# Kernel tuning notes

Hardware: AMD Instinct MI355X
Metric: run time of the kernel (lower is better)

Reference implementation:

```python
import jax, jax.numpy as jnp
import numpy as np

# Graph block sizes (outermost -> innermost), fixed fanout neighbor sampling
N0, N1, N2, N3 = 256000, 25600, 2560, 512
D_IN, D_H, D_OUT = 1024, 256, 19
FANOUTS = (10, 10, 5)


def _lin(key, d_in, d_out):
    return jax.random.normal(key, (d_in, d_out), jnp.float32) / np.sqrt(d_in)


def setup_inputs() -> dict:
    key = jax.random.key(0)
    ks = jax.random.split(key, 13)
    x = jax.random.normal(ks[0], (N0, D_IN), jnp.float32)
    # DGL block convention: dst nodes are the first n_dst src nodes, so
    # h_dst = h[:n_dst]. Neighbor tables index into the src node set.
    nbr0 = jax.random.randint(ks[1], (N1, FANOUTS[0]), 0, N0)
    nbr1 = jax.random.randint(ks[2], (N2, FANOUTS[1]), 0, N1)
    nbr2 = jax.random.randint(ks[3], (N3, FANOUTS[2]), 0, N2)
    return {
        "x": x, "nbr0": nbr0, "nbr1": nbr1, "nbr2": nbr2,
        "Wself0": _lin(ks[4], D_IN, D_H), "Wneigh0": _lin(ks[5], D_IN, D_H),
        "b0": jnp.zeros((D_H,), jnp.float32),
        "Wself1": _lin(ks[6], D_H, D_H), "Wneigh1": _lin(ks[7], D_H, D_H),
        "b1": jnp.zeros((D_H,), jnp.float32),
        "Wself2": _lin(ks[8], D_H, D_OUT), "Wneigh2": _lin(ks[9], D_H, D_OUT),
        "b2": jnp.zeros((D_OUT,), jnp.float32),
    }


def sage_layer(h, nbr, Wself, Wneigh, b):
    # SAGEConv('mean'): fc_self(h_dst) + fc_neigh(mean over sampled neighbors)
    n_dst = nbr.shape[0]
    h_neigh = jnp.mean(h[nbr], axis=1)  # [n_dst, fanout, d] -> [n_dst, d]
    return h[:n_dst] @ Wself + h_neigh @ Wneigh + b


def reference(x, nbr0, nbr1, nbr2,
              Wself0, Wneigh0, b0,
              Wself1, Wneigh1, b1,
              Wself2, Wneigh2, b2):
    # Dropout is identity in eval mode; activation = relu.
    h = jax.nn.relu(sage_layer(x, nbr0, Wself0, Wneigh0, b0))
    h = jax.nn.relu(sage_layer(h, nbr1, Wself1, Wneigh1, b1))
    return sage_layer(h, nbr2, Wself2, Wneigh2, b2)  # [N3, n_classes]
```

## Files before the change

### kernel.cpp

```cpp
#include <hip/hip_runtime.h>
#include <hip/hip_bf16.h>


typedef __attribute__((ext_vector_type(4))) float f32x4;
typedef __attribute__((ext_vector_type(8))) short s16x8;

__device__ __forceinline__ unsigned short f2bf_u16(float f) {
  unsigned int u = __float_as_uint(f);
  u += 0x7fffu + ((u >> 16) & 1u);
  return (unsigned short)(u >> 16);
}

__device__ __forceinline__ float bf2f(unsigned short u) {
  return __uint_as_float(((unsigned int)u) << 16);
}

__global__ void prep_wcat(const float* __restrict__ Wself,
                          const float* __restrict__ Wneigh,
                          unsigned short* __restrict__ Wt, int Khalf, int N) {
  int idx = blockIdx.x * 256 + threadIdx.x;
  int Kc = 2 * Khalf;
  if (idx >= N * Kc) return;
  int n = idx / Kc, k = idx - n * Kc;
  float v = (k < Khalf) ? Wself[(size_t)k * N + n] : Wneigh[(size_t)(k - Khalf) * N + n];
  Wt[idx] = f2bf_u16(v);
}

template <int D, int F>
__global__ void gather_cat(const float* __restrict__ h,
                           const int* __restrict__ nbr,
                           unsigned short* __restrict__ out) {
  const int i = blockIdx.x;
  const int c = threadIdx.x;
  int idx[F];
#pragma unroll
  for (int f = 0; f < F; ++f) idx[f] = nbr[(size_t)i * F + f];
  constexpr float inv = 1.0f / (float)F;

  float4 s = reinterpret_cast<const float4*>(h + (size_t)i * D)[c];
  ushort4 us = {f2bf_u16(s.x), f2bf_u16(s.y), f2bf_u16(s.z), f2bf_u16(s.w)};
  reinterpret_cast<ushort4*>(out + (size_t)i * 2 * D)[c] = us;

  float ax = 0.f, ay = 0.f, az = 0.f, aw = 0.f;
#pragma unroll
  for (int f = 0; f < F; ++f) {
    float4 v = reinterpret_cast<const float4*>(h + (size_t)idx[f] * D)[c];
    ax += v.x; ay += v.y; az += v.z; aw += v.w;
  }
  ushort4 un = {f2bf_u16(ax * inv), f2bf_u16(ay * inv), f2bf_u16(az * inv), f2bf_u16(aw * inv)};
  reinterpret_cast<ushort4*>(out + (size_t)i * 2 * D + D)[c] = un;
}

template <int BM, int BN, int WM, int WN, bool RELU>
__global__ void gemm_bf16(const unsigned short* __restrict__ A,
                          const unsigned short* __restrict__ Bt,
                          const float* __restrict__ bias,
                          float* __restrict__ C,
                          int M, int N, int Kc) {
  constexpr int BK = 32;
  constexpr int LDK = BK + 8;
  constexpr int THREADS = WM * WN * 64;
  constexpr int MF = BM / (WM * 16);
  constexpr int NF = BN / (WN * 16);
  __shared__ __align__(16) unsigned short As[BM][LDK];
  __shared__ __align__(16) unsigned short Bs[BN][LDK];

  const int tid = threadIdx.x;
  const int wid = tid >> 6, lane = tid & 63;
  const int wm = wid / WN, wn = wid % WN;
  const size_t bm = (size_t)blockIdx.x * BM;
  const size_t bn = (size_t)blockIdx.y * BN;

  f32x4 acc[MF][NF];
#pragma unroll
  for (int mi = 0; mi < MF; ++mi)
#pragma unroll
    for (int ni = 0; ni < NF; ++ni)
      acc[mi][ni] = (f32x4){0.f, 0.f, 0.f, 0.f};

  const int arow = tid >> 2;
  const int apart = (tid & 3) * 8;
  const int klo = (lane >> 4) * 8;
  const int l15 = lane & 15;

  for (int kt = 0; kt < Kc; kt += BK) {
#pragma unroll
    for (int r = 0; r < BM; r += THREADS / 4) {
      s16x8 v = *reinterpret_cast<const s16x8*>(A + (bm + r + arow) * (size_t)Kc + kt + apart);
      *reinterpret_cast<s16x8*>(&As[r + arow][apart]) = v;
    }
#pragma unroll
    for (int r = 0; r < BN; r += THREADS / 4) {
      s16x8 v = *reinterpret_cast<const s16x8*>(Bt + (bn + r + arow) * (size_t)Kc + kt + apart);
      *reinterpret_cast<s16x8*>(&Bs[r + arow][apart]) = v;
    }
    __syncthreads();

    s16x8 af[MF], bfr[NF];
#pragma unroll
    for (int mi = 0; mi < MF; ++mi)
      af[mi] = *reinterpret_cast<const s16x8*>(&As[wm * MF * 16 + mi * 16 + l15][klo]);
#pragma unroll
    for (int ni = 0; ni < NF; ++ni)
      bfr[ni] = *reinterpret_cast<const s16x8*>(&Bs[wn * NF * 16 + ni * 16 + l15][klo]);
#pragma unroll
    for (int mi = 0; mi < MF; ++mi)
#pragma unroll
      for (int ni = 0; ni < NF; ++ni)
        acc[mi][ni] = __builtin_amdgcn_mfma_f32_16x16x32_bf16(af[mi], bfr[ni], acc[mi][ni], 0, 0, 0);
    __syncthreads();
  }

  const int rif = (lane >> 4) * 4;
#pragma unroll
  for (int mi = 0; mi < MF; ++mi) {
    size_t r0 = bm + wm * MF * 16 + mi * 16 + rif;
#pragma unroll
    for (int ni = 0; ni < NF; ++ni) {
      int c = (int)bn + wn * NF * 16 + ni * 16 + l15;
      float bv = bias[c];
#pragma unroll
      for (int r = 0; r < 4; ++r) {
        float v = acc[mi][ni][r] + bv;
        if (RELU) v = fmaxf(v, 0.f);
        C[(r0 + r) * (size_t)N + c] = v;
      }
    }
  }
}

__global__ void out_fused(const float* __restrict__ h1, const int* __restrict__ nbr,
                          const float* __restrict__ Ws, const float* __restrict__ Wn,
                          const float* __restrict__ b, float* __restrict__ out) {
  const int i = blockIdx.x, t = threadIdx.x;
  __shared__ float row[512];
  __shared__ float part[8][32];
  row[t] = h1[(size_t)i * 256 + t];
  float s = 0.f;
#pragma unroll
  for (int f = 0; f < 5; ++f) s += h1[(size_t)nbr[i * 5 + f] * 256 + t];
  row[256 + t] = s * 0.2f;
  __syncthreads();
  const int n = t & 31, seg = t >> 5;
  float p = 0.f;
  if (n < 19) {
#pragma unroll
    for (int e = 0; e < 64; ++e) {
      const int k = seg * 64 + e;
      const float w = (k < 256) ? Ws[k * 19 + n] : Wn[(k - 256) * 19 + n];
      p += row[k] * w;
    }
  }
  part[seg][n] = p;
  __syncthreads();
  if (t < 19) {
    float sm = b[t];
#pragma unroll
    for (int g = 0; g < 8; ++g) sm += part[g][t];
    out[(size_t)i * 19 + t] = sm;
  }
}

extern "C" void kernel_launch(void* const* d_in, const int* in_sizes, int n_in,
                              void* d_out, int out_size, void* d_ws, size_t ws_size,
                              hipStream_t stream) {
  const float* x    = (const float*)d_in[0];
  const int*   nbr0 = (const int*)d_in[1];
  const int*   nbr1 = (const int*)d_in[2];
  const int*   nbr2 = (const int*)d_in[3];
  const float* Ws0  = (const float*)d_in[4];
  const float* Wn0  = (const float*)d_in[5];
  const float* b0   = (const float*)d_in[6];
  const float* Ws1  = (const float*)d_in[7];
  const float* Wn1  = (const float*)d_in[8];
  const float* b1   = (const float*)d_in[9];
  const float* Ws2  = (const float*)d_in[10];
  const float* Wn2  = (const float*)d_in[11];
  const float* b2   = (const float*)d_in[12];
  float* out = (float*)d_out;

  char* ws = (char*)d_ws;
  unsigned short* A0   = (unsigned short*)(ws);
  unsigned short* Wt0  = (unsigned short*)(ws + 104857600);
  float*          h0   = (float*)(ws + 105906176);
  unsigned short* cat1 = (unsigned short*)(ws + 132120576);
  unsigned short* Wt1  = (unsigned short*)(ws + 134742016);
  float*          h1   = (float*)(ws + 135004160);

  prep_wcat<<<(256 * 2048 + 255) / 256, 256, 0, stream>>>(Ws0, Wn0, Wt0, 1024, 256);
  prep_wcat<<<(256 * 512 + 255) / 256, 256, 0, stream>>>(Ws1, Wn1, Wt1, 256, 256);

  gather_cat<1024, 10><<<25600, 256, 0, stream>>>(x, nbr0, A0);
  gemm_bf16<64, 256, 1, 4, true>
      <<<dim3(400, 1), 256, 0, stream>>>(A0, Wt0, b0, h0, 25600, 256, 2048);

  gather_cat<256, 10><<<2560, 64, 0, stream>>>(h0, nbr1, cat1);
  gemm_bf16<64, 128, 2, 2, true>
      <<<dim3(40, 2), 256, 0, stream>>>(cat1, Wt1, b1, h1, 2560, 256, 512);

  out_fused<<<512, 256, 0, stream>>>(h1, nbr2, Ws2, Wn2, b2, out);
}
```

Baseline: 310.6 us.

## Rewrite bf16 GEMM with direct global-to-LDS loads, XOR swizzle, BK=64

Replaces the register-staged GEMM with a fixed 64x256 tile kernel that loads A and B straight into LDS with global_load_lds, using an XOR-swizzled layout to avoid bank conflicts and BK=64 to halve the barrier count. The two weight-prep launches are merged into one kernel. The layer-1 GEMM now runs on 40 blocks instead of 80, which lowers parallelism for that small GEMM. The main GEMM still does not double-buffer, so loads and MFMA do not overlap.

Measured after the change: 307.4 us. About the same (-1.0%).

```diff
diff --git a/kernel.cpp b/kernel.cpp
--- a/kernel.cpp
+++ b/kernel.cpp
@@ -11,19 +11,29 @@
   return (unsigned short)(u >> 16);
 }
 
-__device__ __forceinline__ float bf2f(unsigned short u) {
-  return __uint_as_float(((unsigned int)u) << 16);
-}
-
-__global__ void prep_wcat(const float* __restrict__ Wself,
-                          const float* __restrict__ Wneigh,
-                          unsigned short* __restrict__ Wt, int Khalf, int N) {
+__device__ __forceinline__ void gload16(const void* g, void* l) {
+  __builtin_amdgcn_global_load_lds(
+      (const __attribute__((address_space(1))) unsigned int*)g,
+      (__attribute__((address_space(3))) unsigned int*)l, 16, 0, 0);
+}
+
+__global__ void prep_wcat2(const float* __restrict__ Ws0, const float* __restrict__ Wn0,
+                           unsigned short* __restrict__ Wt0,
+                           const float* __restrict__ Ws1, const float* __restrict__ Wn1,
+                           unsigned short* __restrict__ Wt1) {
   int idx = blockIdx.x * 256 + threadIdx.x;
-  int Kc = 2 * Khalf;
-  if (idx >= N * Kc) return;
-  int n = idx / Kc, k = idx - n * Kc;
-  float v = (k < Khalf) ? Wself[(size_t)k * N + n] : Wneigh[(size_t)(k - Khalf) * N + n];
-  Wt[idx] = f2bf_u16(v);
+  if (idx < 256 * 2048) {
+    int n = idx >> 11, k = idx & 2047;
+    float v = (k < 1024) ? Ws0[k * 256 + n] : Wn0[(k - 1024) * 256 + n];
+    Wt0[idx] = f2bf_u16(v);
+  } else {
+    int i2 = idx - 256 * 2048;
+    if (i2 < 256 * 512) {
+      int n = i2 >> 9, k = i2 & 511;
+      float v = (k < 256) ? Ws1[k * 256 + n] : Wn1[(k - 256) * 256 + n];
+      Wt1[i2] = f2bf_u16(v);
+    }
+  }
 }
 
 template <int D, int F>
@@ -51,79 +61,82 @@
   reinterpret_cast<ushort4*>(out + (size_t)i * 2 * D + D)[c] = un;
 }
 
-template <int BM, int BN, int WM, int WN, bool RELU>
-__global__ void gemm_bf16(const unsigned short* __restrict__ A,
-                          const unsigned short* __restrict__ Bt,
-                          const float* __restrict__ bias,
-                          float* __restrict__ C,
-                          int M, int N, int Kc) {
-  constexpr int BK = 32;
-  constexpr int LDK = BK + 8;
-  constexpr int THREADS = WM * WN * 64;
-  constexpr int MF = BM / (WM * 16);
-  constexpr int NF = BN / (WN * 16);
-  __shared__ __align__(16) unsigned short As[BM][LDK];
-  __shared__ __align__(16) unsigned short Bs[BN][LDK];
+template <bool RELU>
+__global__ __launch_bounds__(256) void gemm_gl(
+    const unsigned short* __restrict__ A,
+    const unsigned short* __restrict__ Bt,
+    const float* __restrict__ bias,
+    float* __restrict__ C,
+    int Kc) {
+  constexpr int BM = 64, BN = 256, BK = 64;
+  __shared__ __align__(16) unsigned short As[BM * BK];
+  __shared__ __align__(16) unsigned short Bs[BN * BK];
 
   const int tid = threadIdx.x;
   const int wid = tid >> 6, lane = tid & 63;
-  const int wm = wid / WN, wn = wid % WN;
   const size_t bm = (size_t)blockIdx.x * BM;
-  const size_t bn = (size_t)blockIdx.y * BN;
-
-  f32x4 acc[MF][NF];
-#pragma unroll
-  for (int mi = 0; mi < MF; ++mi)
-#pragma unroll
-    for (int ni = 0; ni < NF; ++ni)
+
+  const int srow = (wid << 3) + (lane >> 3);
+  const int gs = (lane & 7) ^ ((lane >> 3) & 7);
+  const unsigned short* gA = A + (bm + srow) * (size_t)Kc + gs * 8;
+  const unsigned short* gB = Bt + (size_t)srow * Kc + gs * 8;
+  unsigned short* lA = As + wid * 512;
+  unsigned short* lB = Bs + wid * 512;
+
+  f32x4 acc[4][4];
+#pragma unroll
+  for (int mi = 0; mi < 4; ++mi)
+#pragma unroll
+    for (int ni = 0; ni < 4; ++ni)
       acc[mi][ni] = (f32x4){0.f, 0.f, 0.f, 0.f};
 
-  const int arow = tid >> 2;
-  const int apart = (tid & 3) * 8;
-  const int klo = (lane >> 4) * 8;
-  const int l15 = lane & 15;
+  const int l15 = lane & 15, lq = lane >> 4, l7 = lane & 7;
 
   for (int kt = 0; kt < Kc; kt += BK) {
-#pragma unroll
-    for (int r = 0; r < BM; r += THREADS / 4) {
-      s16x8 v = *reinterpret_cast<const s16x8*>(A + (bm + r + arow) * (size_t)Kc + kt + apart);
-      *reinterpret_cast<s16x8*>(&As[r + arow][apart]) = v;
-    }
-#pragma unroll
-    for (int r = 0; r < BN; r += THREADS / 4) {
-      s16x8 v = *reinterpret_cast<const s16x8*>(Bt + (bn + r + arow) * (size_t)Kc + kt + apart);
-      *reinterpret_cast<s16x8*>(&Bs[r + arow][apart]) = v;
-    }
+    gload16(gA + kt, lA);
+    gload16(gA + 32 * (size_t)Kc + kt, lA + 2048);
+#pragma unroll
+    for (int p = 0; p < 8; ++p)
+      gload16(gB + p * 32 * (size_t)Kc + kt, lB + p * 2048);
     __syncthreads();
 
-    s16x8 af[MF], bfr[NF];
-#pragma unroll
-    for (int mi = 0; mi < MF; ++mi)
-      af[mi] = *reinterpret_cast<const s16x8*>(&As[wm * MF * 16 + mi * 16 + l15][klo]);
-#pragma unroll
-    for (int ni = 0; ni < NF; ++ni)
-      bfr[ni] = *reinterpret_cast<const s16x8*>(&Bs[wn * NF * 16 + ni * 16 + l15][klo]);
-#pragma unroll
-    for (int mi = 0; mi < MF; ++mi)
-#pragma unroll
-      for (int ni = 0; ni < NF; ++ni)
-        acc[mi][ni] = __builtin_amdgcn_mfma_f32_16x16x32_bf16(af[mi], bfr[ni], acc[mi][ni], 0, 0, 0);
+#pragma unroll
+    for (int ks = 0; ks < 2; ++ks) {
+      const int gr = ((ks << 2) + lq) ^ l7;
+      s16x8 af[4], bf_[4];
+#pragma unroll
+      for (int mi = 0; mi < 4; ++mi) {
+        const int row = mi * 16 + l15;
+        af[mi] = *reinterpret_cast<const s16x8*>(
+            reinterpret_cast<const char*>(As) + row * 128 + gr * 16);
+      }
+#pragma unroll
+      for (int ni = 0; ni < 4; ++ni) {
+        const int row = wid * 64 + ni * 16 + l15;
+        bf_[ni] = *reinterpret_cast<const s16x8*>(
+            reinterpret_cast<const char*>(Bs) + row * 128 + gr * 16);
+      }
+#pragma unroll
+      for (int mi = 0; mi < 4; ++mi)
+#pragma unroll
+        for (int ni = 0; ni < 4; ++ni)
+          acc[mi][ni] = __builtin_amdgcn_mfma_f32_16x16x32_bf16(af[mi], bf_[ni], acc[mi][ni], 0, 0, 0);
+    }
     __syncthreads();
   }
 
-  const int rif = (lane >> 4) * 4;
-#pragma unroll
-  for (int mi = 0; mi < MF; ++mi) {
-    size_t r0 = bm + wm * MF * 16 + mi * 16 + rif;
-#pragma unroll
-    for (int ni = 0; ni < NF; ++ni) {
-      int c = (int)bn + wn * NF * 16 + ni * 16 + l15;
-      float bv = bias[c];
-#pragma unroll
-      for (int r = 0; r < 4; ++r) {
-        float v = acc[mi][ni][r] + bv;
+#pragma unroll
+  for (int mi = 0; mi < 4; ++mi) {
+    const size_t r0 = bm + mi * 16 + lq * 4;
+#pragma unroll
+    for (int ni = 0; ni < 4; ++ni) {
+      const int c = wid * 64 + ni * 16 + l15;
+      const float bv = bias[c];
+#pragma unroll
+      for (int rr = 0; rr < 4; ++rr) {
+        float v = acc[mi][ni][rr] + bv;
         if (RELU) v = fmaxf(v, 0.f);
-        C[(r0 + r) * (size_t)N + c] = v;
+        C[(r0 + rr) * (size_t)BN + c] = v;
       }
     }
   }
@@ -187,16 +200,14 @@
   unsigned short* Wt1  = (unsigned short*)(ws + 134742016);
   float*          h1   = (float*)(ws + 135004160);
 
-  prep_wcat<<<(256 * 2048 + 255) / 256, 256, 0, stream>>>(Ws0, Wn0, Wt0, 1024, 256);
-  prep_wcat<<<(256 * 512 + 255) / 256, 256, 0, stream>>>(Ws1, Wn1, Wt1, 256, 256);
+  prep_wcat2<<<(256 * 2048 + 256 * 512 + 255) / 256, 256, 0, stream>>>(
+      Ws0, Wn0, Wt0, Ws1, Wn1, Wt1);
 
   gather_cat<1024, 10><<<25600, 256, 0, stream>>>(x, nbr0, A0);
-  gemm_bf16<64, 256, 1, 4, true>
-      <<<dim3(400, 1), 256, 0, stream>>>(A0, Wt0, b0, h0, 25600, 256, 2048);
+  gemm_gl<true><<<400, 256, 0, stream>>>(A0, Wt0, b0, h0, 2048);
 
   gather_cat<256, 10><<<2560, 64, 0, stream>>>(h0, nbr1, cat1);
-  gemm_bf16<64, 128, 2, 2, true>
-      <<<dim3(40, 2), 256, 0, stream>>>(cat1, Wt1, b1, h1, 2560, 256, 512);
+  gemm_gl<true><<<40, 256, 0, stream>>>(cat1, Wt1, b1, h1, 512);
 
   out_fused<<<512, 256, 0, stream>>>(h1, nbr2, Ws2, Wn2, b2, out);
 }
```
